# Performance work log

Measured on AMD Instinct MI355X. Metric: run time of the kernel, lower is better.

The kernel has to match this reference:

```python
import jax, jax.numpy as jnp
import numpy as np

DIM = 512
HEADS = 8
DIM_HEAD = 64
INNER = HEADS * DIM_HEAD  # 512
NARROW_K = 9
WIDE_K = 9
WIDE_DIL = 5


def setup_inputs() -> dict:
    key = jax.random.key(0)
    ks = jax.random.split(key, 12)
    b, n = 4, 2048
    s = lambda fan_in: 1.0 / np.sqrt(fan_in)
    inp = {
        'tokens': jax.random.normal(ks[0], (b, n, DIM), jnp.float32),
        'mask': jax.random.randint(ks[1], (b, n), 0, 2) > 0,
        'w_qkv': jax.random.normal(ks[2], (DIM, INNER * 3), jnp.float32) * s(DIM),
        'w_out': jax.random.normal(ks[3], (INNER, DIM), jnp.float32) * s(INNER),
        'b_out': jnp.zeros((DIM,), jnp.float32),
        'w_narrow': jax.random.normal(ks[4], (DIM, DIM, NARROW_K), jnp.float32) * s(DIM * NARROW_K),
        'b_narrow': jnp.zeros((DIM,), jnp.float32),
        'w_wide': jax.random.normal(ks[5], (DIM, DIM, WIDE_K), jnp.float32) * s(DIM * WIDE_K),
        'b_wide': jnp.zeros((DIM,), jnp.float32),
        'ln1_g': jnp.ones((DIM,), jnp.float32),
        'ln1_b': jnp.zeros((DIM,), jnp.float32),
        'ff_w': jax.random.normal(ks[6], (DIM, DIM), jnp.float32) * s(DIM),
        'ff_b': jnp.zeros((DIM,), jnp.float32),
        'ln2_g': jnp.ones((DIM,), jnp.float32),
        'ln2_b': jnp.zeros((DIM,), jnp.float32),
    }
    return inp


def layer_norm(x, g, b, eps=1e-5):
    m = jnp.mean(x, axis=-1, keepdims=True)
    v = jnp.mean(jnp.square(x - m), axis=-1, keepdims=True)
    return (x - m) / jnp.sqrt(v + eps) * g + b


def rope_encoding(seq_len, dim_head, dtype):
    inv_freq = 1.0 / (10000.0 ** (jnp.arange(0, dim_head, 2, dtype=jnp.float32) / dim_head))
    pos = jnp.arange(seq_len, dtype=jnp.float32)
    sinu = jnp.einsum('i,j->ij', pos, inv_freq)  # [n, d/2]
    return jnp.concatenate([jnp.sin(sinu), jnp.cos(sinu)], axis=-1).astype(dtype)  # [n, d]


def attn(tokens, mask, w_qkv, w_out, b_out):
    b, n, _ = tokens.shape
    qkv = tokens @ w_qkv  # [b, n, 3*inner]
    q, k, v = jnp.split(qkv, 3, axis=-1)
    reshp = lambda t: t.reshape(b, n, HEADS, DIM_HEAD).transpose(0, 2, 1, 3)  # b h n d
    q, k, v = reshp(q), reshp(k), reshp(v)
    rope = rope_encoding(n, DIM_HEAD, tokens.dtype)  # [n, d]
    q = q + rope
    k = k + rope
    mask4 = mask[:, None, :, None]  # b 1 n 1
    big = jnp.finfo(k.dtype).max
    k = jnp.where(mask4, k, -big)
    q = jax.nn.softmax(q, axis=-1) * (DIM_HEAD ** -0.5)
    k = jax.nn.softmax(k, axis=2)  # over n
    v = jnp.where(mask4, v, 0.0)
    context = jnp.einsum('bhnd,bhne->bhde', k, v)
    out = jnp.einsum('bhde,bhnd->bhne', context, q)
    out = out.transpose(0, 2, 1, 3).reshape(b, n, INNER)
    return out @ w_out + b_out


def conv1d(x, w, b, padding, dilation):
    # x: [b, c, n], w: [out, in, k]
    y = jax.lax.conv_general_dilated(
        x, w, window_strides=(1,), padding=[(padding, padding)],
        rhs_dilation=(dilation,), dimension_numbers=('NCW', 'OIW', 'NCW'))
    return y + b[None, :, None]


def reference(tokens, mask, w_qkv, w_out, b_out, w_narrow, b_narrow,
              w_wide, b_wide, ln1_g, ln1_b, ff_w, ff_b, ln2_g, ln2_b):
    tokens = attn(tokens, mask, w_qkv, w_out, b_out)
    conv_in = tokens.transpose(0, 2, 1)  # b d n
    conv_in = jnp.where(mask[:, None, :], conv_in, 0.0)
    narrow = jax.nn.gelu(conv1d(conv_in, w_narrow, b_narrow, NARROW_K // 2, 1), approximate=False)
    wide_pad = (WIDE_K + (WIDE_K - 1) * (WIDE_DIL - 1)) // 2  # 20
    wide = jax.nn.gelu(conv1d(conv_in, w_wide, b_wide, wide_pad, WIDE_DIL), approximate=False)
    tokens = tokens + narrow.transpose(0, 2, 1) + wide.transpose(0, 2, 1)
    tokens = layer_norm(tokens, ln1_g, ln1_b)
    tokens = layer_norm(jax.nn.gelu(tokens @ ff_w + ff_b, approximate=False), ln2_g, ln2_b)
    return tokens
```

## Files before the change

### kernel.cpp

```cpp
#include <hip/hip_runtime.h>
#include <hip/hip_bf16.h>

#define BB 4
#define NN 2048
#define NROWS (BB*NN)

typedef unsigned short u16;
typedef __bf16 bf16x8 __attribute__((ext_vector_type(8)));
typedef u16    u16x8  __attribute__((ext_vector_type(8)));
typedef float  fx4    __attribute__((ext_vector_type(4)));

__device__ __forceinline__ float bf2f(u16 u){
  union { float f; unsigned int i; } x; x.i = ((unsigned int)u) << 16; return x.f;
}
__device__ __forceinline__ u16 f2bf(float f){
  union { float f; unsigned int i; } x; x.f = f;
  unsigned int i = x.i;
  i += 0x7fffu + ((i >> 16) & 1u);
  return (u16)(i >> 16);
}
__device__ __forceinline__ float geluf(float x){
  return 0.5f * x * (1.0f + erff(x * 0.70710678118654752f));
}
__device__ __forceinline__ void gload16(const void* g, void* l){
  __builtin_amdgcn_global_load_lds((const __attribute__((address_space(1))) unsigned int*)g,
                                   (__attribute__((address_space(3))) unsigned int*)l, 16, 0, 0);
}

__global__ __launch_bounds__(256) void sniff_k(const u16* tokens, const unsigned int* mask, int* flags){
  __shared__ int s_f32, s_byte;
  if (threadIdx.x == 0) { s_f32 = 0; s_byte = 0; }
  __syncthreads();
  for (int i = threadIdx.x; i < 4096; i += 256) {
    float v = bf2f(tokens[i]);
    if (!(fabsf(v) < 1e10f)) atomicOr(&s_f32, 1);
  }
  for (int i = threadIdx.x; i < 2048; i += 256) {
    if (mask[i] > 1u) atomicOr(&s_byte, 1);
  }
  __syncthreads();
  if (threadIdx.x == 0) { flags[0] = s_f32; flags[1] = s_byte; }
}

__global__ __launch_bounds__(256) void misc_k(const void* mask, const void* tokens,
                                              const void* p0, const void* p1, const void* p2,
                                              const void* p3, const void* p4, const void* p5,
                                              const void* p6, const void* p7,
                                              const int* flags, float* rope, int* m32,
                                              float* params, float* ctx, float* kS, u16* tokbf){
  const void* srcs[8] = {p0,p1,p2,p3,p4,p5,p6,p7};
  int f32 = flags[0], mbyte = flags[1];
  const int T = 131072 + 8192 + 4096 + 131072 + 2048 + 4194304;
  for (int i = blockIdx.x*256 + threadIdx.x; i < T; i += gridDim.x*256) {
    if (i < 131072) {
      int p = i >> 6, j = i & 63;
      int jj = (j < 32) ? j : j - 32;
      float invf = exp2f(-(float)jj * (13.287712379549449f/32.0f));
      float prod = (float)p * invf;
      rope[i] = (j < 32) ? sinf(prod) : cosf(prod);
    } else if (i < 139264) {
      int k = i - 131072;
      int v = mbyte ? (int)((const unsigned char*)mask)[k] : ((const int*)mask)[k];
      m32[k] = v ? 1 : 0;
    } else if (i < 143360) {
      int k = i - 139264;
      int pid = k >> 9, j = k & 511;
      const void* s = srcs[pid];
      params[k] = f32 ? ((const float*)s)[j] : bf2f(((const u16*)s)[j]);
    } else if (i < 274432) {
      ctx[i - 143360] = 0.0f;
    } else if (i < 276480) {
      kS[i - 274432] = 0.0f;
    } else {
      int k = i - 276480;
      tokbf[k] = f32 ? f2bf(((const float*)tokens)[k]) : ((const u16*)tokens)[k];
    }
  }
}

__global__ __launch_bounds__(256) void prep2_k(const void* w_qkv, const void* w_out, const void* ff_w,
                                               const void* w_narrow, const void* w_wide,
                                               const int* flags,
                                               u16* wqkvt, u16* woutt, u16* ffwt,
                                               u16* wtN2, u16* wtW2){
  int bid = blockIdx.x;
  int f = flags[0];
  int tid = threadIdx.x;
  if (bid < 1024) {
    int tensor = bid >> 9, o = bid & 511;
    const void* src = tensor ? w_wide : w_narrow;
    u16* dst = tensor ? wtW2 : wtN2;
    __shared__ u16 Ls[4608];
    for (int i = tid; i < 4608; i += 256) {
      Ls[i] = f ? f2bf(((const float*)src)[(size_t)o*4608 + i]) : ((const u16*)src)[(size_t)o*4608 + i];
    }
    __syncthreads();
    #pragma unroll
    for (int kk = 0; kk < 9; kk++) {
      #pragma unroll
      for (int u = 0; u < 2; u++) {
        int c = tid + u*256;
        dst[(size_t)kk*262144 + o*512 + c] = Ls[c*9 + kk];
      }
    }
  } else {
    int id = bid - 1024;
    int z = id / 192;
    int rem = id - z*192;
    int x = rem % 24, y = rem / 24;
    int Nn = (z == 0) ? 1536 : 512;
    if (x * 64 >= Nn) return;
    const void* src = (z == 0) ? w_qkv : (z == 1) ? w_out : ff_w;
    u16* dst = (z == 0) ? wqkvt : (z == 1) ? woutt : ffwt;
    __shared__ u16 Ts[64][72];
    int n0 = x * 64, k0 = y * 64;
    int r = tid >> 2, cq = (tid & 3) * 16;
    #pragma unroll
    for (int u = 0; u < 2; u++) {
      int c = cq + u*8;
      int sidx = (k0 + r)*Nn + n0 + c;
      u16x8 v;
      if (f) {
        #pragma unroll
        for (int j = 0; j < 8; j++) v[j] = f2bf(((const float*)src)[sidx + j]);
      } else {
        v = *(const u16x8*)&((const u16*)src)[sidx];
      }
      *(u16x8*)&Ts[r][c] = v;
    }
    __syncthreads();
    #pragma unroll
    for (int u = 0; u < 2; u++) {
      int c = cq + u*8;
      u16x8 v;
      #pragma unroll
      for (int j = 0; j < 8; j++) v[j] = Ts[c + j][r];
      *(u16x8*)&dst[(size_t)(n0 + r)*512 + k0 + c] = v;
    }
  }
}

__global__ __launch_bounds__(256) void mgemm_qkv_k(const u16* A, const u16* Bt, const float* rope,
                                                   const int* mask, u16* qb, u16* keb, u16* vb){
  __shared__ u16 As[128][40];
  __shared__ u16 Bs[128][40];
  __shared__ int smask[128];
  int tid = threadIdx.x;
  int lane = tid & 63;
  int wave = tid >> 6;
  int wm = (wave >> 1) * 64, wn = (wave & 1) * 64;
  int quad = lane >> 4, l16 = lane & 15;
  int m0 = blockIdx.y * 128, n0 = blockIdx.x * 128;
  fx4 acc[4][4] = {};
  int ar = tid >> 2;
  int ac = (tid & 3) * 8;
  for (int k0 = 0; k0 < 512; k0 += 32) {
    *(u16x8*)&As[ar][ac]    = *(const u16x8*)&A[(size_t)(m0+ar)*512 + k0 + ac];
    *(u16x8*)&As[ar+64][ac] = *(const u16x8*)&A[(size_t)(m0+ar+64)*512 + k0 + ac];
    *(u16x8*)&Bs[ar][ac]    = *(const u16x8*)&Bt[(size_t)(n0+ar)*512 + k0 + ac];
    *(u16x8*)&Bs[ar+64][ac] = *(const u16x8*)&Bt[(size_t)(n0+ar+64)*512 + k0 + ac];
    __syncthreads();
    bf16x8 af[4], bfv[4];
    #pragma unroll
    for (int i = 0; i < 4; i++)
      af[i] = __builtin_bit_cast(bf16x8, *(const u16x8*)&As[wm + i*16 + l16][quad*8]);
    #pragma unroll
    for (int j = 0; j < 4; j++)
      bfv[j] = __builtin_bit_cast(bf16x8, *(const u16x8*)&Bs[wn + j*16 + l16][quad*8]);
    #pragma unroll
    for (int i = 0; i < 4; i++)
      #pragma unroll
      for (int j = 0; j < 4; j++)
        acc[i][j] = __builtin_amdgcn_mfma_f32_16x16x32_bf16(af[i], bfv[j], acc[i][j], 0, 0, 0);
    __syncthreads();
  }
  int x = blockIdx.x;
  if (x >= 4) {
    if (tid < 128) smask[tid] = mask[m0 + tid];
    __syncthreads();
  }
  if (x < 4) {
    #pragma unroll
    for (int i = 0; i < 4; i++)
      #pragma unroll
      for (int r = 0; r < 4; r++) {
        int rl = wm + i*16 + quad*4 + r;
        int row = m0 + rl;
        int nseq = row & (NN-1);
        const float* rp = rope + nseq*64 + l16;
        float e0 = __expf(acc[i][0][r] + rp[0]);
        float e1 = __expf(acc[i][1][r] + rp[16]);
        float e2 = __expf(acc[i][2][r] + rp[32]);
        float e3 = __expf(acc[i][3][r] + rp[48]);
        float s = e0 + e1 + e2 + e3;
        s += __shfl_xor(s, 1); s += __shfl_xor(s, 2);
        s += __shfl_xor(s, 4); s += __shfl_xor(s, 8);
        float sc = 0.125f / s;
        size_t base = (size_t)row*512 + n0 + wn + l16;
        qb[base]      = f2bf(e0*sc);
        qb[base + 16] = f2bf(e1*sc);
        qb[base + 32] = f2bf(e2*sc);
        qb[base + 48] = f2bf(e3*sc);
      }
  } else if (x < 8) {
    #pragma unroll
    for (int i = 0; i < 4; i++)
      #pragma unroll
      for (int r = 0; r < 4; r++) {
        int rl = wm + i*16 + quad*4 + r;
        int row = m0 + rl;
        int nseq = row & (NN-1);
        int mk = smask[rl];
        const float* rp = rope + nseq*64 + l16;
        size_t base = (size_t)row*512 + (n0 - 512) + wn + l16;
        #pragma unroll
        for (int j = 0; j < 4; j++) {
          float ke = mk ? __expf(acc[i][j][r] + rp[j*16]) : 0.0f;
          keb[base + j*16] = f2bf(ke);
        }
      }
  } else {
    #pragma unroll
    for (int i = 0; i < 4; i++)
      #pragma unroll
      for (int r = 0; r < 4; r++) {
        int rl = wm + i*16 + quad*4 + r;
        int row = m0 + rl;
        int mk = smask[rl];
        size_t base = (size_t)row*512 + (n0 - 1024) + wn + l16;
        #pragma unroll
        for (int j = 0; j < 4; j++)
          vb[base + j*16] = mk ? f2bf(acc[i][j][r]) : (u16)0;
      }
  }
}

#define FMA16(a, b, acc) \
  acc[0][0] = fmaf(a.x, b.x, acc[0][0]); acc[0][1] = fmaf(a.x, b.y, acc[0][1]); \
  acc[0][2] = fmaf(a.x, b.z, acc[0][2]); acc[0][3] = fmaf(a.x, b.w, acc[0][3]); \
  acc[1][0] = fmaf(a.y, b.x, acc[1][0]); acc[1][1] = fmaf(a.y, b.y, acc[1][1]); \
  acc[1][2] = fmaf(a.y, b.z, acc[1][2]); acc[1][3] = fmaf(a.y, b.w, acc[1][3]); \
  acc[2][0] = fmaf(a.z, b.x, acc[2][0]); acc[2][1] = fmaf(a.z, b.y, acc[2][1]); \
  acc[2][2] = fmaf(a.z, b.z, acc[2][2]); acc[2][3] = fmaf(a.z, b.w, acc[2][3]); \
  acc[3][0] = fmaf(a.w, b.x, acc[3][0]); acc[3][1] = fmaf(a.w, b.y, acc[3][1]); \
  acc[3][2] = fmaf(a.w, b.z, acc[3][2]); acc[3][3] = fmaf(a.w, b.w, acc[3][3]);

__global__ __launch_bounds__(256) void ctx_k(const u16* keb, const u16* vb, float* ctx, float* Sg){
  int bh = blockIdx.x, seg = blockIdx.y;
  int b = bh >> 3, h = bh & 7;
  __shared__ float Ks[32][68], Vs[32][68];
  __shared__ float sS[64];
  int tid = threadIdx.x, tx = tid & 15, ty = tid >> 4;
  if (tid < 64) sS[tid] = 0.0f;
  float acc[4][4] = {{0.f,0.f,0.f,0.f},{0.f,0.f,0.f,0.f},{0.f,0.f,0.f,0.f},{0.f,0.f,0.f,0.f}};
  float sp[8] = {0,0,0,0,0,0,0,0};
  int nl = tid >> 3, dcol = (tid & 7)*8;
  const u16* kp0 = keb + (size_t)(b*NN + seg*256)*512 + h*64 + dcol;
  const u16* vp0 = vb  + (size_t)(b*NN + seg*256)*512 + h*64 + dcol;
  for (int nc = 0; nc < 256; nc += 32) {
    u16x8 ku = *(const u16x8*)(kp0 + (size_t)(nc + nl)*512);
    u16x8 vu = *(const u16x8*)(vp0 + (size_t)(nc + nl)*512);
    float a[8], bb[8];
    #pragma unroll
    for (int t = 0; t < 8; t++) { a[t] = bf2f(ku[t]); bb[t] = bf2f(vu[t]); sp[t] += a[t]; }
    *(float4*)&Ks[nl][dcol]   = (float4){a[0],a[1],a[2],a[3]};
    *(float4*)&Ks[nl][dcol+4] = (float4){a[4],a[5],a[6],a[7]};
    *(float4*)&Vs[nl][dcol]   = (float4){bb[0],bb[1],bb[2],bb[3]};
    *(float4*)&Vs[nl][dcol+4] = (float4){bb[4],bb[5],bb[6],bb[7]};
    __syncthreads();
    #pragma unroll
    for (int q = 0; q < 32; q++) {
      float4 a4 = *(const float4*)&Ks[q][ty*4];
      float4 b4 = *(const float4*)&Vs[q][tx*4];
      FMA16(a4, b4, acc)
    }
    __syncthreads();
  }
  #pragma unroll
  for (int j = 0; j < 8; j++) atomicAdd(&sS[dcol + j], sp[j]);
  float* cp = ctx + (size_t)bh*4096;
  #pragma unroll
  for (int i = 0; i < 4; i++)
    #pragma unroll
    for (int j = 0; j < 4; j++)
      atomicAdd(&cp[(ty*4 + i)*64 + tx*4 + j], acc[i][j]);
  __syncthreads();
  if (tid < 64) atomicAdd(&Sg[bh*64 + tid], sS[tid]);
}

__global__ __launch_bounds__(256) void ctxw_k(const float* ctx, const float* Sg, const u16* woutt,
                                              u16* W2t, u16* cpadb){
  int bx = blockIdx.x;
  int tid = threadIdx.x;
  if (bx >= 32) {
    int idx = (bx - 32)*256 + tid;
    if (idx < BB*40*512) {
      int c = idx & 511;
      int t = (idx >> 9) % 40;
      int b = idx / (40*512);
      int tt = (t < 20) ? t : 2048 + t;
      cpadb[((size_t)b*2088 + tt)*512 + c] = 0;
    }
    return;
  }
  int h = bx & 7, b = bx >> 3;
  int lane = tid & 63, wave = tid >> 6;
  int quad = lane >> 4, l16 = lane & 15;
  const float* cp = ctx + (size_t)(b*8 + h)*4096;
  fx4 acc[8][4] = {};
  #pragma unroll
  for (int ks = 0; ks < 2; ks++) {
    bf16x8 bfv[4];
    #pragma unroll
    for (int j = 0; j < 4; j++) {
      int d = j*16 + l16;
      float S = Sg[(b*8 + h)*64 + d];
      float rs = (S > 0.0f) ? 1.0f/S : 0.0f;
      const float* src = cp + d*64 + ks*32 + quad*8;
      float4 v0 = *(const float4*)src, v1 = *(const float4*)(src + 4);
      bf16x8 t;
      t[0]=(__bf16)(v0.x*rs); t[1]=(__bf16)(v0.y*rs); t[2]=(__bf16)(v0.z*rs); t[3]=(__bf16)(v0.w*rs);
      t[4]=(__bf16)(v1.x*rs); t[5]=(__bf16)(v1.y*rs); t[6]=(__bf16)(v1.z*rs); t[7]=(__bf16)(v1.w*rs);
      bfv[j] = t;
    }
    #pragma unroll
    for (int i = 0; i < 8; i++) {
      int orow = wave*128 + i*16 + l16;
      bf16x8 afr = __builtin_bit_cast(bf16x8, *(const u16x8*)&woutt[(size_t)orow*512 + h*64 + ks*32 + quad*8]);
      #pragma unroll
      for (int j = 0; j < 4; j++)
        acc[i][j] = __builtin_amdgcn_mfma_f32_16x16x32_bf16(afr, bfv[j], acc[i][j], 0, 0, 0);
    }
  }
  u16* out = W2t + (size_t)b*262144;
  #pragma unroll
  for (int i = 0; i < 8; i++)
    #pragma unroll
    for (int j = 0; j < 4; j++)
      #pragma unroll
      for (int r = 0; r < 4; r++) {
        int orow = wave*128 + i*16 + quad*4 + r;
        out[(size_t)orow*512 + h*64 + j*16 + l16] = f2bf(acc[i][j][r]);
      }
}

__global__ __launch_bounds__(256) void mgemm_attn64_k(const u16* qb, const u16* W2t, const float* bias,
                                                      const int* mask, u16* attnb, u16* cpadb){
  __shared__ u16 As[64][40];
  __shared__ u16 Bs[128][40];
  int tid = threadIdx.x;
  int lane = tid & 63;
  int wave = tid >> 6;
  int wn = wave * 32;
  int quad = lane >> 4, l16 = lane & 15;
  int m0 = blockIdx.y * 64, n0 = blockIdx.x * 128, b = blockIdx.z;
  const u16* A  = qb  + (size_t)b*2048*512;
  const u16* Bt = W2t + (size_t)b*262144;
  fx4 acc[4][2] = {};
  int ar = tid >> 2;
  int ac = (tid & 3) * 8;
  for (int k0 = 0; k0 < 512; k0 += 32) {
    *(u16x8*)&As[ar][ac]    = *(const u16x8*)&A[(size_t)(m0+ar)*512 + k0 + ac];
    *(u16x8*)&Bs[ar][ac]    = *(const u16x8*)&Bt[(size_t)(n0+ar)*512 + k0 + ac];
    *(u16x8*)&Bs[ar+64][ac] = *(const u16x8*)&Bt[(size_t)(n0+ar+64)*512 + k0 + ac];
    __syncthreads();
    bf16x8 af[4], bfv[2];
    #pragma unroll
    for (int i = 0; i < 4; i++)
      af[i] = __builtin_bit_cast(bf16x8, *(const u16x8*)&As[i*16 + l16][quad*8]);
    #pragma unroll
    for (int j = 0; j < 2; j++)
      bfv[j] = __builtin_bit_cast(bf16x8, *(const u16x8*)&Bs[wn + j*16 + l16][quad*8]);
    #pragma unroll
    for (int i = 0; i < 4; i++)
      #pragma unroll
      for (int j = 0; j < 2; j++)
        acc[i][j] = __builtin_amdgcn_mfma_f32_16x16x32_bf16(af[i], bfv[j], acc[i][j], 0, 0, 0);
    __syncthreads();
  }
  #pragma unroll
  for (int i = 0; i < 4; i++)
    #pragma unroll
    for (int j = 0; j < 2; j++) {
      int col = n0 + wn + j*16 + l16;
      float bv = bias[col];
      #pragma unroll
      for (int r = 0; r < 4; r++) {
        int row_l = m0 + i*16 + quad*4 + r;
        float v = acc[i][j][r] + bv;
        u16 vbb = f2bf(v);
        attnb[((size_t)b*2048 + row_l)*512 + col] = vbb;
        int mk = mask[b*2048 + row_l];
        cpadb[((size_t)b*2088 + row_l + 20)*512 + col] = mk ? vbb : (u16)0;
      }
    }
}

__global__ __launch_bounds__(256, 2) void mconv8_k(const u16* cpad, const u16* Wn, const u16* Ww,
                                                   const float* bias_n, const float* bias_w,
                                                   u16* Dn, u16* Dw){
  __shared__ u16 As[296*32];
  __shared__ u16 Ws[9*64*32];
  int tid = threadIdx.x;
  int lane = tid & 63;
  int wave = tid >> 6;
  int wm = wave * 64;
  int quad = lane >> 4, l16 = lane & 15;
  int o0 = blockIdx.x * 64, m0 = blockIdx.y * 256;
  int b = blockIdx.z >> 1, cid = blockIdx.z & 1;
  const u16* W = cid ? Ww : Wn;
  const float* bias = cid ? bias_w : bias_n;
  u16* D = cid ? Dw : Dn;
  fx4 acc[4][4] = {};
  const u16* cb = cpad + ((size_t)b*2088 + m0)*512;
  int w_o   = tid >> 2;
  int w_lsl = ((tid & 3) ^ ((tid >> 3) & 3)) * 8;
  int wslot = ((quad ^ ((l16 >> 1) & 3)) * 8);
  for (int c0 = 0; c0 < 512; c0 += 32) {
    __syncthreads();
    #pragma unroll
    for (int it = 0; it < 5; it++) {
      int s = it*256 + tid;
      if (s < 1184) {
        int row = s >> 2;
        int lsl = ((s & 3) ^ ((s >> 3) & 3)) * 8;
        gload16(&cb[(size_t)row*512 + c0 + lsl], &As[(it*256 + wave*64)*8]);
      }
    }
    #pragma unroll
    for (int it = 0; it < 9; it++) {
      gload16(&W[(size_t)it*262144 + (size_t)(o0 + w_o)*512 + c0 + w_lsl],
              &Ws[(it*256 + wave*64)*8]);
    }
    __syncthreads();
    #pragma unroll
    for (int kk = 0; kk < 9; kk++) {
      int shift = cid ? 5*kk : 16 + kk;
      int rowb = shift + wm + l16;
      int aslot = ((quad ^ ((rowb >> 1) & 3)) * 8);
      bf16x8 bfv[4];
      #pragma unroll
      for (int j = 0; j < 4; j++)
        bfv[j] = __builtin_bit_cast(bf16x8, *(const u16x8*)&Ws[(kk*64 + j*16 + l16)*32 + wslot]);
      #pragma unroll
      for (int i = 0; i < 4; i++) {
        bf16x8 afr = __builtin_bit_cast(bf16x8, *(const u16x8*)&As[(rowb + i*16)*32 + aslot]);
        #pragma unroll
        for (int j = 0; j < 4; j++)
          acc[i][j] = __builtin_amdgcn_mfma_f32_16x16x32_bf16(afr, bfv[j], acc[i][j], 0, 0, 0);
      }
    }
  }
  #pragma unroll
  for (int i = 0; i < 4; i++)
    #pragma unroll
    for (int j = 0; j < 4; j++) {
      int col = o0 + j*16 + l16;
      float bv = bias[col];
      #pragma unroll
      for (int r = 0; r < 4; r++) {
        int row = b*2048 + m0 + wm + i*16 + quad*4 + r;
        D[(size_t)row*512 + col] = f2bf(geluf(acc[i][j][r] + bv));
      }
    }
}

template<bool BIAS, bool GELU>
__global__ __launch_bounds__(256) void mgemm64b_k(const u16* A, const u16* Bt, const float* bias,
                                                  u16* C, int M, int N, int K){
  __shared__ u16 As[64][40];
  __shared__ u16 Bs[128][40];
  int tid = threadIdx.x;
  int lane = tid & 63;
  int wave = tid >> 6;
  int wn = wave * 32;
  int quad = lane >> 4, l16 = lane & 15;
  int m0 = blockIdx.y * 64, n0 = blockIdx.x * 128;
  fx4 acc[4][2] = {};
  int ar = tid >> 2;
  int ac = (tid & 3) * 8;
  for (int k0 = 0; k0 < K; k0 += 32) {
    *(u16x8*)&As[ar][ac]    = *(const u16x8*)&A[(size_t)(m0+ar)*K + k0 + ac];
    *(u16x8*)&Bs[ar][ac]    = *(const u16x8*)&Bt[(size_t)(n0+ar)*K + k0 + ac];
    *(u16x8*)&Bs[ar+64][ac] = *(const u16x8*)&Bt[(size_t)(n0+ar+64)*K + k0 + ac];
    __syncthreads();
    bf16x8 af[4], bfv[2];
    #pragma unroll
    for (int i = 0; i < 4; i++)
      af[i] = __builtin_bit_cast(bf16x8, *(const u16x8*)&As[i*16 + l16][quad*8]);
    #pragma unroll
    for (int j = 0; j < 2; j++)
      bfv[j] = __builtin_bit_cast(bf16x8, *(const u16x8*)&Bs[wn + j*16 + l16][quad*8]);
    #pragma unroll
    for (int i = 0; i < 4; i++)
      #pragma unroll
      for (int j = 0; j < 2; j++)
        acc[i][j] = __builtin_amdgcn_mfma_f32_16x16x32_bf16(af[i], bfv[j], acc[i][j], 0, 0, 0);
    __syncthreads();
  }
  #pragma unroll
  for (int i = 0; i < 4; i++)
    #pragma unroll
    for (int j = 0; j < 2; j++) {
      int col = n0 + wn + j*16 + l16;
      float bv = BIAS ? bias[col] : 0.0f;
      #pragma unroll
      for (int r = 0; r < 4; r++) {
        int row = m0 + i*16 + quad*4 + r;
        float v = acc[i][j][r] + bv;
        if (GELU) v = geluf(v);
        C[(size_t)row*N + col] = f2bf(v);
      }
    }
}

__device__ __forceinline__ float block_sum512(float v, float* red){
  #pragma unroll
  for (int o = 32; o; o >>= 1) v += __shfl_xor(v, o, 64);
  int w = threadIdx.x >> 6;
  if ((threadIdx.x & 63) == 0) red[w] = v;
  __syncthreads();
  float t = red[0] + red[1] + red[2] + red[3];
  __syncthreads();
  return t;
}

template<int NADD, int OM>
__global__ __launch_bounds__(256) void ln_k(const u16* X, const u16* Y, const u16* Z,
                                            const float* g, const float* be,
                                            const int* flags, void* out){
  __shared__ float red[4];
  size_t row = blockIdx.x;
  int tid = threadIdx.x;
  const u16* xp = X + row*512;
  float x0 = bf2f(xp[tid]), x1 = bf2f(xp[tid + 256]);
  if (NADD >= 1) { const u16* yp = Y + row*512; x0 += bf2f(yp[tid]); x1 += bf2f(yp[tid + 256]); }
  if (NADD >= 2) { const u16* zp = Z + row*512; x0 += bf2f(zp[tid]); x1 += bf2f(zp[tid + 256]); }
  float mean = block_sum512(x0 + x1, red) * (1.0f/512.0f);
  float d0 = x0 - mean, d1 = x1 - mean;
  float var = block_sum512(d0*d0 + d1*d1, red) * (1.0f/512.0f);
  float inv = rsqrtf(var + 1e-5f);
  float r0 = d0*inv*g[tid]       + be[tid];
  float r1 = d1*inv*g[tid + 256] + be[tid + 256];
  bool obf = (OM == 1) || (OM == 2 && !flags[0]);
  if (obf) {
    u16* op = (u16*)out;
    op[row*512 + tid]       = f2bf(r0);
    op[row*512 + tid + 256] = f2bf(r1);
  } else {
    float* op = (float*)out;
    op[row*512 + tid]       = r0;
    op[row*512 + tid + 256] = r1;
  }
}

extern "C" void kernel_launch(void* const* d_in, const int* in_sizes, int n_in,
                              void* d_out, int out_size, void* d_ws, size_t ws_size,
                              hipStream_t stream) {
  const void* tokens   = d_in[0];
  const void* mask     = d_in[1];
  const void* w_qkv    = d_in[2];
  const void* w_out    = d_in[3];
  const void* b_out    = d_in[4];
  const void* w_narrow = d_in[5];
  const void* b_narrow = d_in[6];
  const void* w_wide   = d_in[7];
  const void* b_wide   = d_in[8];
  const void* ln1_g    = d_in[9];
  const void* ln1_b    = d_in[10];
  const void* ff_w     = d_in[11];
  const void* ff_b     = d_in[12];
  const void* ln2_g    = d_in[13];
  const void* ln2_b    = d_in[14];

  float* ws = (float*)d_ws;
  int*   flags  = (int*)ws;
  int*   m32    = (int*)(ws + 16);
  float* params = ws + 8208;
  float* kS     = ws + 12304;
  float* ctx    = ws + 14352;
  float* rope   = ws + 145424;
  u16*   tokbf  = (u16*)(ws + 276496);
  u16*   wqkvt  = (u16*)(ws + 2373648);
  u16*   woutt  = (u16*)(ws + 2766864);
  u16*   ffwt   = (u16*)(ws + 2897936);
  u16*   wtN2   = (u16*)(ws + 3029008);
  u16*   wtW2   = (u16*)(ws + 4208656);
  u16*   qb     = (u16*)(ws + 5388304);
  u16*   keb    = (u16*)(ws + 7485456);
  u16*   vb     = (u16*)(ws + 9582608);
  u16*   W2t    = (u16*)(ws + 11679760);
  u16*   attnb  = (u16*)(ws + 12204048);
  u16*   cpadb  = (u16*)(ws + 14301200);
  u16*   Dnb    = (u16*)(ws + 16439312);
  u16*   Dwb    = (u16*)(ws + 18536464);
  u16*   Eb     = attnb;
  u16*   t1b    = tokbf;

  float* p_bout = params;        float* p_bnar = params + 512;
  float* p_bwid = params + 1024; float* p_l1g  = params + 1536;
  float* p_l1b  = params + 2048; float* p_ffb  = params + 2560;
  float* p_l2g  = params + 3072; float* p_l2b  = params + 3584;

  sniff_k<<<dim3(1), dim3(256), 0, stream>>>((const u16*)tokens, (const unsigned int*)mask, flags);
  misc_k<<<dim3(8192), dim3(256), 0, stream>>>(mask, tokens, b_out, b_narrow, b_wide, ln1_g, ln1_b,
                                               ff_b, ln2_g, ln2_b, flags, rope, m32, params, ctx,
                                               kS, tokbf);
  prep2_k<<<dim3(1600), dim3(256), 0, stream>>>(w_qkv, w_out, ff_w, w_narrow, w_wide, flags,
                                                wqkvt, woutt, ffwt, wtN2, wtW2);

  mgemm_qkv_k<<<dim3(12, 64), dim3(256), 0, stream>>>(
      tokbf, wqkvt, rope, m32, qb, keb, vb);

  ctx_k<<<dim3(32, 8), dim3(256), 0, stream>>>(keb, vb, ctx, kS);

  ctxw_k<<<dim3(352), dim3(256), 0, stream>>>(ctx, kS, woutt, W2t, cpadb);

  mgemm_attn64_k<<<dim3(4, 32, 4), dim3(256), 0, stream>>>(qb, W2t, p_bout, m32, attnb, cpadb);

  mconv8_k<<<dim3(8, 8, 8), dim3(256), 0, stream>>>(cpadb, wtN2, wtW2, p_bnar, p_bwid, Dnb, Dwb);

  ln_k<2,1><<<dim3(NROWS), dim3(256), 0, stream>>>(attnb, Dnb, Dwb, p_l1g, p_l1b, flags, (void*)t1b);

  mgemm64b_k<true,true><<<dim3(4, 128), dim3(256), 0, stream>>>(
      t1b, ffwt, p_ffb, Eb, NROWS, 512, 512);

  ln_k<0,2><<<dim3(NROWS), dim3(256), 0, stream>>>(Eb, nullptr, nullptr, p_l2g, p_l2b, flags, d_out);
}
```

Measured before the change: 379.6 us.

## Double-buffer LDS tiles in dual conv kernel to overlap loads with MFMA

Converts the fused narrow/wide convolution kernel to a double-buffered LDS scheme. The next 32-channel slice of activations and weights is prefetched into the alternate buffer while MFMAs run on the current one, leaving one barrier per iteration instead of two. This is meant to hide global-to-LDS load latency. In exchange LDS use doubles (about 112 KB per block) and the occupancy hint of 2 blocks per CU is dropped, which may reduce occupancy.

```diff
diff --git a/kernel.cpp b/kernel.cpp
--- a/kernel.cpp
+++ b/kernel.cpp
@@ -396,11 +396,13 @@
     }
 }
 
-__global__ __launch_bounds__(256, 2) void mconv8_k(const u16* cpad, const u16* Wn, const u16* Ww,
-                                                   const float* bias_n, const float* bias_w,
-                                                   u16* Dn, u16* Dw){
-  __shared__ u16 As[296*32];
-  __shared__ u16 Ws[9*64*32];
+#define A_SZ (296*32)
+#define W_SZ (9*64*32)
+__global__ __launch_bounds__(256) void mconv9_k(const u16* cpad, const u16* Wn, const u16* Ww,
+                                                const float* bias_n, const float* bias_w,
+                                                u16* Dn, u16* Dw){
+  __shared__ u16 As[2*A_SZ];
+  __shared__ u16 Ws[2*W_SZ];
   int tid = threadIdx.x;
   int lane = tid & 63;
   int wave = tid >> 6;
@@ -416,23 +418,47 @@
   int w_o   = tid >> 2;
   int w_lsl = ((tid & 3) ^ ((tid >> 3) & 3)) * 8;
   int wslot = ((quad ^ ((l16 >> 1) & 3)) * 8);
-  for (int c0 = 0; c0 < 512; c0 += 32) {
-    __syncthreads();
+
+  {
     #pragma unroll
     for (int it = 0; it < 5; it++) {
       int s = it*256 + tid;
       if (s < 1184) {
         int row = s >> 2;
         int lsl = ((s & 3) ^ ((s >> 3) & 3)) * 8;
-        gload16(&cb[(size_t)row*512 + c0 + lsl], &As[(it*256 + wave*64)*8]);
+        gload16(&cb[(size_t)row*512 + lsl], &As[(it*256 + wave*64)*8]);
       }
     }
     #pragma unroll
     for (int it = 0; it < 9; it++) {
-      gload16(&W[(size_t)it*262144 + (size_t)(o0 + w_o)*512 + c0 + w_lsl],
+      gload16(&W[(size_t)it*262144 + (size_t)(o0 + w_o)*512 + w_lsl],
               &Ws[(it*256 + wave*64)*8]);
     }
-    __syncthreads();
+  }
+  __syncthreads();
+
+  for (int ch = 0; ch < 16; ch++) {
+    int cur = ch & 1;
+    if (ch < 15) {
+      int c0 = (ch + 1) * 32;
+      int nb = cur ^ 1;
+      #pragma unroll
+      for (int it = 0; it < 5; it++) {
+        int s = it*256 + tid;
+        if (s < 1184) {
+          int row = s >> 2;
+          int lsl = ((s & 3) ^ ((s >> 3) & 3)) * 8;
+          gload16(&cb[(size_t)row*512 + c0 + lsl], &As[nb*A_SZ + (it*256 + wave*64)*8]);
+        }
+      }
+      #pragma unroll
+      for (int it = 0; it < 9; it++) {
+        gload16(&W[(size_t)it*262144 + (size_t)(o0 + w_o)*512 + c0 + w_lsl],
+                &Ws[nb*W_SZ + (it*256 + wave*64)*8]);
+      }
+    }
+    const u16* Asb = &As[cur*A_SZ];
+    const u16* Wsb = &Ws[cur*W_SZ];
     #pragma unroll
     for (int kk = 0; kk < 9; kk++) {
       int shift = cid ? 5*kk : 16 + kk;
@@ -441,15 +467,16 @@
       bf16x8 bfv[4];
       #pragma unroll
       for (int j = 0; j < 4; j++)
-        bfv[j] = __builtin_bit_cast(bf16x8, *(const u16x8*)&Ws[(kk*64 + j*16 + l16)*32 + wslot]);
+        bfv[j] = __builtin_bit_cast(bf16x8, *(const u16x8*)&Wsb[(kk*64 + j*16 + l16)*32 + wslot]);
       #pragma unroll
       for (int i = 0; i < 4; i++) {
-        bf16x8 afr = __builtin_bit_cast(bf16x8, *(const u16x8*)&As[(rowb + i*16)*32 + aslot]);
+        bf16x8 afr = __builtin_bit_cast(bf16x8, *(const u16x8*)&Asb[(rowb + i*16)*32 + aslot]);
         #pragma unroll
         for (int j = 0; j < 4; j++)
           acc[i][j] = __builtin_amdgcn_mfma_f32_16x16x32_bf16(afr, bfv[j], acc[i][j], 0, 0, 0);
       }
     }
+    __syncthreads();
   }
   #pragma unroll
   for (int i = 0; i < 4; i++)
@@ -618,7 +645,7 @@
 
   mgemm_attn64_k<<<dim3(4, 32, 4), dim3(256), 0, stream>>>(qb, W2t, p_bout, m32, attnb, cpadb);
 
-  mconv8_k<<<dim3(8, 8, 8), dim3(256), 0, stream>>>(cpadb, wtN2, wtW2, p_bnar, p_bwid, Dnb, Dwb);
+  mconv9_k<<<dim3(8, 8, 8), dim3(256), 0, stream>>>(cpadb, wtN2, wtW2, p_bnar, p_bwid, Dnb, Dwb);
 
   ln_k<2,1><<<dim3(NROWS), dim3(256), 0, stream>>>(attnb, Dnb, Dwb, p_l1g, p_l1b, flags, (void*)t1b);
 
```

Result: faster. 369.7 us (-2.6%).

## Double-buffer conv kernel LDS stages and enlarge block to 512 threads

Applied to the files above, without the earlier changes.

The dilated/narrow conv GEMM kernel now uses 512-thread blocks covering 512 rows, so the 9 weight taps are shared across twice as many rows. Its A and W LDS tiles are double-buffered so the next channel chunk's global-to-LDS loads are issued while MFMAs run on the current chunk, and only one barrier is kept per iteration. The cost is roughly 2x LDS use (about 2*(552+576)*32*2 bytes), which lowers occupancy to likely one block per CU, and a grid of only 256 blocks.

```diff
diff --git a/kernel.cpp b/kernel.cpp
--- a/kernel.cpp
+++ b/kernel.cpp
@@ -396,43 +396,64 @@
     }
 }
 
-__global__ __launch_bounds__(256, 2) void mconv8_k(const u16* cpad, const u16* Wn, const u16* Ww,
-                                                   const float* bias_n, const float* bias_w,
-                                                   u16* Dn, u16* Dw){
-  __shared__ u16 As[296*32];
-  __shared__ u16 Ws[9*64*32];
+#define A_ROWS 552
+#define A_SZ (A_ROWS*32)
+#define W_SZ (9*64*32)
+__global__ __launch_bounds__(512) void mconv10_k(const u16* cpad, const u16* Wn, const u16* Ww,
+                                                 const float* bias_n, const float* bias_w,
+                                                 u16* Dn, u16* Dw){
+  __shared__ u16 As[2*A_SZ];
+  __shared__ u16 Ws[2*W_SZ];
   int tid = threadIdx.x;
   int lane = tid & 63;
   int wave = tid >> 6;
   int wm = wave * 64;
   int quad = lane >> 4, l16 = lane & 15;
-  int o0 = blockIdx.x * 64, m0 = blockIdx.y * 256;
+  int o0 = blockIdx.x * 64, m0 = blockIdx.y * 512;
   int b = blockIdx.z >> 1, cid = blockIdx.z & 1;
   const u16* W = cid ? Ww : Wn;
   const float* bias = cid ? bias_w : bias_n;
   u16* D = cid ? Dw : Dn;
   fx4 acc[4][4] = {};
   const u16* cb = cpad + ((size_t)b*2088 + m0)*512;
-  int w_o   = tid >> 2;
-  int w_lsl = ((tid & 3) ^ ((tid >> 3) & 3)) * 8;
   int wslot = ((quad ^ ((l16 >> 1) & 3)) * 8);
-  for (int c0 = 0; c0 < 512; c0 += 32) {
-    __syncthreads();
-    #pragma unroll
-    for (int it = 0; it < 5; it++) {
-      int s = it*256 + tid;
-      if (s < 1184) {
-        int row = s >> 2;
-        int lsl = ((s & 3) ^ ((s >> 3) & 3)) * 8;
-        gload16(&cb[(size_t)row*512 + c0 + lsl], &As[(it*256 + wave*64)*8]);
-      }
-    }
-    #pragma unroll
-    for (int it = 0; it < 9; it++) {
-      gload16(&W[(size_t)it*262144 + (size_t)(o0 + w_o)*512 + c0 + w_lsl],
-              &Ws[(it*256 + wave*64)*8]);
-    }
-    __syncthreads();
+
+#define STAGE_CHUNK(c0, buf)                                                          \
+  {                                                                                   \
+    _Pragma("unroll")                                                                 \
+    for (int it = 0; it < 5; it++) {                                                  \
+      int s = it*512 + tid;                                                           \
+      if (s < 2208) {                                                                 \
+        int lsl = ((s & 3) ^ ((s >> 3) & 3)) * 8;                                     \
+        gload16(&cb[(size_t)(s >> 2)*512 + (c0) + lsl],                               \
+                &As[(buf)*A_SZ + (it*512 + wave*64)*8]);                              \
+      }                                                                               \
+    }                                                                                 \
+    _Pragma("unroll")                                                                 \
+    for (int it = 0; it < 5; it++) {                                                  \
+      int s = it*512 + tid;                                                           \
+      if (s < 2304) {                                                                 \
+        int kk = s >> 8;                                                              \
+        int ow = (s >> 2) & 63;                                                       \
+        int lsl = ((s & 3) ^ ((s >> 3) & 3)) * 8;                                     \
+        gload16(&W[(size_t)kk*262144 + (size_t)(o0 + ow)*512 + (c0) + lsl],           \
+                &Ws[(buf)*W_SZ + (it*512 + wave*64)*8]);                              \
+      }                                                                               \
+    }                                                                                 \
+  }
+
+  STAGE_CHUNK(0, 0)
+  __syncthreads();
+
+  for (int ch = 0; ch < 16; ch++) {
+    int cur = ch & 1;
+    if (ch < 15) {
+      int c0n = (ch + 1) * 32;
+      int nb = cur ^ 1;
+      STAGE_CHUNK(c0n, nb)
+    }
+    const u16* Asb = &As[cur*A_SZ];
+    const u16* Wsb = &Ws[cur*W_SZ];
     #pragma unroll
     for (int kk = 0; kk < 9; kk++) {
       int shift = cid ? 5*kk : 16 + kk;
@@ -441,16 +462,18 @@
       bf16x8 bfv[4];
       #pragma unroll
       for (int j = 0; j < 4; j++)
-        bfv[j] = __builtin_bit_cast(bf16x8, *(const u16x8*)&Ws[(kk*64 + j*16 + l16)*32 + wslot]);
+        bfv[j] = __builtin_bit_cast(bf16x8, *(const u16x8*)&Wsb[(kk*64 + j*16 + l16)*32 + wslot]);
       #pragma unroll
       for (int i = 0; i < 4; i++) {
-        bf16x8 afr = __builtin_bit_cast(bf16x8, *(const u16x8*)&As[(rowb + i*16)*32 + aslot]);
+        bf16x8 afr = __builtin_bit_cast(bf16x8, *(const u16x8*)&Asb[(rowb + i*16)*32 + aslot]);
         #pragma unroll
         for (int j = 0; j < 4; j++)
           acc[i][j] = __builtin_amdgcn_mfma_f32_16x16x32_bf16(afr, bfv[j], acc[i][j], 0, 0, 0);
       }
     }
-  }
+    __syncthreads();
+  }
+#undef STAGE_CHUNK
   #pragma unroll
   for (int i = 0; i < 4; i++)
     #pragma unroll
@@ -618,7 +641,7 @@
 
   mgemm_attn64_k<<<dim3(4, 32, 4), dim3(256), 0, stream>>>(qb, W2t, p_bout, m32, attnb, cpadb);
 
-  mconv8_k<<<dim3(8, 8, 8), dim3(256), 0, stream>>>(cpadb, wtN2, wtW2, p_bnar, p_bwid, Dnb, Dwb);
+  mconv10_k<<<dim3(8, 4, 8), dim3(512), 0, stream>>>(cpadb, wtN2, wtW2, p_bnar, p_bwid, Dnb, Dwb);
 
   ln_k<2,1><<<dim3(NROWS), dim3(256), 0, stream>>>(attnb, Dnb, Dwb, p_l1g, p_l1b, flags, (void*)t1b);
 
```

Result: faster. 335.0 us (-11.7%).
